# Optimization experiments

Hardware: AMD Instinct MI355X
Metric: run time of the kernel (lower is better)

## Reference

```python
import jax, jax.numpy as jnp
import numpy as np

B, S, D, H, F, E, K = 4, 2048, 1024, 16, 4096, 8, 2
HD = D // H
TEMP = 1.0
EPS = 1e-5


def _layernorm(x, g, b):
    mu = jnp.mean(x, axis=-1, keepdims=True)
    var = jnp.mean((x - mu) ** 2, axis=-1, keepdims=True)
    return (x - mu) * jax.lax.rsqrt(var + EPS) * g + b


def setup_inputs() -> dict:
    key = jax.random.key(0)
    ks = jax.random.split(key, 20)
    sd = 1.0 / np.sqrt(D)
    sf = 1.0 / np.sqrt(F)
    inp = {
        'x': jax.random.normal(ks[0], (B, S, D), jnp.float32),
        'Wq': jax.random.normal(ks[1], (D, D), jnp.float32) * sd,
        'bq': jnp.zeros((D,), jnp.float32),
        'Wk': jax.random.normal(ks[2], (D, D), jnp.float32) * sd,
        'bk': jnp.zeros((D,), jnp.float32),
        'Wv': jax.random.normal(ks[3], (D, D), jnp.float32) * sd,
        'bv': jnp.zeros((D,), jnp.float32),
        'Wo': jax.random.normal(ks[4], (D, D), jnp.float32) * sd,
        'bo': jnp.zeros((D,), jnp.float32),
        'g1': jnp.ones((D,), jnp.float32),
        'beta1': jnp.zeros((D,), jnp.float32),
        'gateW': jax.random.normal(ks[5], (D, E), jnp.float32) * sd,
        'gateb': jnp.zeros((E,), jnp.float32),
        'eW1': jax.random.normal(ks[6], (E, D, F), jnp.float32) * sd,
        'eb1': jnp.zeros((E, F), jnp.float32),
        'eW2': jax.random.normal(ks[7], (E, F, D), jnp.float32) * sf,
        'eb2': jnp.zeros((E, D), jnp.float32),
        'g2': jnp.ones((D,), jnp.float32),
        'beta2': jnp.zeros((D,), jnp.float32),
    }
    return inp


def _forward(x, Wq, bq, Wk, bk, Wv, bv, Wo, bo, g1, beta1, gateW, gateb, eW1, eb1, eW2, eb2, g2, beta2):
    # ---- multi-head self-attention ----
    q = (x @ Wq + bq).reshape(B, S, H, HD).transpose(0, 2, 1, 3)  # [B,H,S,HD]
    k = (x @ Wk + bk).reshape(B, S, H, HD).transpose(0, 2, 1, 3)
    v = (x @ Wv + bv).reshape(B, S, H, HD).transpose(0, 2, 1, 3)
    scores = jnp.einsum('bhqd,bhkd->bhqk', q, k) / np.sqrt(HD)
    attn = jax.nn.softmax(scores, axis=-1)
    out = jnp.einsum('bhqk,bhkd->bhqd', attn, v)
    out = out.transpose(0, 2, 1, 3).reshape(B, S, D) @ Wo + bo
    x = _layernorm(x + out, g1, beta1)

    # ---- MoE feed-forward with top-k routing ----
    T = B * S
    xf = x.reshape(T, D)
    gate_logits = (xf @ gateW + gateb) / TEMP
    gate_scores = jax.nn.softmax(gate_logits, axis=-1)            # [T,E]
    topk_scores, topk_idx = jax.lax.top_k(gate_scores, K)         # [T,K]
    topk_scores = topk_scores / jnp.sum(topk_scores, axis=-1, keepdims=True)
    # per-token combine weight for every expert: [T,E]
    w_full = jnp.zeros((T, E), xf.dtype).at[jnp.arange(T)[:, None], topk_idx].add(topk_scores)
    moe_out = jnp.zeros_like(xf)
    for e in range(E):  # small fixed expert count
        h = jax.nn.gelu(xf @ eW1[e] + eb1[e], approximate=False)
        y = h @ eW2[e] + eb2[e]
        moe_out = moe_out + w_full[:, e:e + 1] * y

    # ---- load-balancing auxiliary loss ----
    counts = jnp.sum(jax.nn.one_hot(topk_idx, E, dtype=xf.dtype), axis=(0, 1))  # [E]
    expert_fraction = counts / (T * K)
    routing_weights = jnp.mean(gate_scores, axis=0)
    aux_loss = E * jnp.sum(expert_fraction * routing_weights)

    x = _layernorm(x + moe_out.reshape(B, S, D), g2, beta2)
    return x, aux_loss


def reference(x, Wq, bq, Wk, bk, Wv, bv, Wo, bo, g1, beta1, gateW, gateb, eW1, eb1, eW2, eb2, g2, beta2):
    return _forward(x, Wq, bq, Wk, bk, Wv, bv, Wo, bo, g1, beta1, gateW, gateb, eW1, eb1, eW2, eb2, g2, beta2)
```

## Files before the change

### kernel.cpp

```cpp
#include <hip/hip_runtime.h>
#include <math.h>

typedef unsigned short u16;
typedef __attribute__((ext_vector_type(8))) u16 u16x8;
typedef __attribute__((ext_vector_type(8))) __bf16 b16x8;
typedef __attribute__((ext_vector_type(4))) float f32x4;

#define DEV __device__ __forceinline__

namespace {

constexpr int Tc = 8192, Dc = 1024, Fc = 4096, Ec = 8;

DEV u16 f2bf(float f){ union{float f; unsigned u;} v; v.f=f; unsigned r = v.u + 0x7fffu + ((v.u>>16)&1u); return (u16)(r>>16); }
DEV float bf2f(u16 h){ union{unsigned u; float f;} v; v.u=((unsigned)h)<<16; return v.f; }
DEV f32x4 zero4(){ f32x4 z = {0.f,0.f,0.f,0.f}; return z; }
DEV f32x4 mfma16(u16x8 a, u16x8 b, f32x4 c){
  union { u16x8 u; b16x8 b; } ua, ub; ua.u = a; ub.u = b;
  return __builtin_amdgcn_mfma_f32_16x16x32_bf16(ua.b, ub.b, c, 0, 0, 0);
}
DEV float gelu_exact(float v){ return 0.5f*v*(1.0f + erff(v*0.70710678118654752f)); }

__global__ __launch_bounds__(256) void split_x_k(const float* __restrict__ x, u16* __restrict__ hi, u16* __restrict__ lo){
  size_t i = (size_t)blockIdx.x*256 + threadIdx.x;
  #pragma unroll
  for (int r=0;r<8;r++){
    size_t idx = i + (size_t)r*1048576;
    float v = x[idx];
    u16 h = f2bf(v);
    hi[idx] = h;
    lo[idx] = f2bf(v - bf2f(h));
  }
}

__global__ __launch_bounds__(256) void concat_bias_k(const float* __restrict__ bq, const float* __restrict__ bk,
                                                     const float* __restrict__ bv, float* __restrict__ dst){
  int n = blockIdx.x*256 + threadIdx.x;
  if (n < 3072) dst[n] = (n<1024) ? bq[n] : ((n<2048) ? bk[n-1024] : bv[n-2048]);
}

__global__ __launch_bounds__(256) void transpose_split_k(const float* __restrict__ W, u16* __restrict__ oHi, u16* __restrict__ oLo,
                                                         int Kd, int Nd, size_t inStride, size_t outStride){
  __shared__ float t[32][33];
  int e = blockIdx.z;
  W += (size_t)e*inStride; oHi += (size_t)e*outStride; if (oLo) oLo += (size_t)e*outStride;
  int k0 = blockIdx.x*32, n0 = blockIdx.y*32;
  int c = threadIdx.x & 31, r0 = threadIdx.x >> 5;
  #pragma unroll
  for (int i=0;i<4;i++){ int r = r0 + i*8; t[r][c] = W[(size_t)(k0+r)*Nd + n0 + c]; }
  __syncthreads();
  #pragma unroll
  for (int i=0;i<4;i++){
    int r = r0 + i*8;
    float v = t[c][r];
    size_t oidx = (size_t)(n0+r)*Kd + k0 + c;
    u16 h = f2bf(v);
    oHi[oidx] = h;
    if (oLo) oLo[oidx] = f2bf(v - bf2f(h));
  }
}

template<int MODE>
__global__ __launch_bounds__(256,2) void gemm_k(
    const u16* __restrict__ Ahi, const u16* __restrict__ Alo,
    const u16* __restrict__ Bhi, const u16* __restrict__ Blo,
    const float* __restrict__ bias,
    float* __restrict__ outF, u16* __restrict__ outHi, u16* __restrict__ outLo,
    const int* __restrict__ offsets,
    int N, int K, int lda, int ldb)
{
  constexpr bool X3 = (MODE <= 1);
  constexpr int PL = X3 ? 2 : 1;
  int Me = 0, rowbase = 0;
  if constexpr (MODE >= 2){
    int e = blockIdx.z;
    rowbase = offsets[e];
    Me = offsets[e+1] - rowbase;
    if ((int)blockIdx.x*128 >= Me) return;
    Ahi += (size_t)rowbase * lda;
    Bhi += (size_t)e * N * K;
    bias += (size_t)e * N;
  }
  __shared__ u16 sA[PL][128*40];
  __shared__ u16 sB[PL][128*40];
  const int tid = threadIdx.x;
  const int lane = tid & 63, wid = tid >> 6;
  const int l15 = lane & 15, l4 = lane >> 4;
  const int mh = (wid >> 1) * 64, nh = (wid & 1) * 64;
  const int bm = blockIdx.x, bn = blockIdx.y;

  f32x4 acc[4][4];
  #pragma unroll
  for (int i=0;i<4;i++)
    #pragma unroll
    for (int j=0;j<4;j++) acc[i][j] = zero4();

  const int nK = K >> 5;
  for (int kb=0; kb<nK; ++kb){
    const int k0 = kb << 5;
    __syncthreads();
    #pragma unroll
    for (int r2=0;r2<2;r2++){
      int c = tid + r2*256;
      int row = c >> 2, k8 = (c & 3) * 8;
      size_t ga = (size_t)(bm*128 + row)*lda + k0 + k8;
      size_t gb = (size_t)(bn*128 + row)*ldb + k0 + k8;
      *(u16x8*)&sA[0][row*40 + k8] = *(const u16x8*)(Ahi + ga);
      *(u16x8*)&sB[0][row*40 + k8] = *(const u16x8*)(Bhi + gb);
      if constexpr (X3){
        *(u16x8*)&sA[1][row*40 + k8] = *(const u16x8*)(Alo + ga);
        *(u16x8*)&sB[1][row*40 + k8] = *(const u16x8*)(Blo + gb);
      }
    }
    __syncthreads();
    u16x8 af[PL][4], bfr[PL][4];
    #pragma unroll
    for (int mt=0;mt<4;mt++){
      int ra = (mh + mt*16 + l15)*40 + l4*8;
      int rb = (nh + mt*16 + l15)*40 + l4*8;
      af[0][mt]  = *(const u16x8*)&sA[0][ra];
      bfr[0][mt] = *(const u16x8*)&sB[0][rb];
      if constexpr (X3){ af[1][mt] = *(const u16x8*)&sA[1][ra]; bfr[1][mt] = *(const u16x8*)&sB[1][rb]; }
    }
    #pragma unroll
    for (int mt=0;mt<4;mt++)
      #pragma unroll
      for (int nt=0;nt<4;nt++){
        acc[mt][nt] = mfma16(af[0][mt], bfr[0][nt], acc[mt][nt]);
        if constexpr (X3){
          acc[mt][nt] = mfma16(af[0][mt], bfr[1][nt], acc[mt][nt]);
          acc[mt][nt] = mfma16(af[1][mt], bfr[0][nt], acc[mt][nt]);
        }
      }
  }
  #pragma unroll
  for (int mt=0;mt<4;mt++)
    #pragma unroll
    for (int nt=0;nt<4;nt++)
      #pragma unroll
      for (int r=0;r<4;r++){
        int m = bm*128 + mh + mt*16 + l4*4 + r;
        int n = bn*128 + nh + nt*16 + l15;
        float v = acc[mt][nt][r];
        if constexpr (MODE == 0){
          v += bias[n];
          int which = n >> 10, h = (n >> 6) & 15, d = n & 63;
          int b = m >> 11, s = m & 2047;
          size_t idx = ((((size_t)which*4 + b)*16 + h)*2048 + s)*64 + d;
          u16 hi = f2bf(v);
          outHi[idx] = hi; outLo[idx] = f2bf(v - bf2f(hi));
        } else if constexpr (MODE == 1){
          outF[(size_t)m*1024 + n] = v + bias[n];
        } else if constexpr (MODE == 2){
          if (m < Me){
            float g = gelu_exact(v + bias[n]);
            outHi[(size_t)(rowbase + m)*N + n] = f2bf(g);
          }
        } else {
          if (m < Me){
            outHi[(size_t)(rowbase + m)*N + n] = f2bf(v + bias[n]);
          }
        }
      }
}

__global__ __launch_bounds__(256,2) void flash_k(
    const u16* __restrict__ qhi, const u16* __restrict__ qlo,
    const u16* __restrict__ khi, const u16* __restrict__ klo,
    const u16* __restrict__ vhi, const u16* __restrict__ vlo,
    u16* __restrict__ ohi, u16* __restrict__ olo)
{
  __shared__ u16 Kl[2][64*72];
  __shared__ u16 Vt[2][64*72];
  __shared__ u16 Pl[2][64*72];
  const int qt = blockIdx.x, bh = blockIdx.y;
  const int b = bh >> 4, h = bh & 15;
  const int tid = threadIdx.x, wid = tid >> 6, lane = tid & 63;
  const int l15 = lane & 15, l4 = lane >> 4;
  const size_t bhBase = (size_t)bh * (2048*64);

  u16x8 qf[2][2];
  #pragma unroll
  for (int ks=0;ks<2;ks++){
    size_t po = bhBase + (size_t)(qt*64 + wid*16 + l15)*64 + ks*32 + l4*8;
    qf[0][ks] = *(const u16x8*)(qhi + po);
    qf[1][ks] = *(const u16x8*)(qlo + po);
  }
  f32x4 O[4];
  #pragma unroll
  for (int nd=0;nd<4;nd++) O[nd] = zero4();
  float mrow[4], lrow[4];
  #pragma unroll
  for (int r=0;r<4;r++){ mrow[r] = -1e30f; lrow[r] = 0.f; }

  for (int t=0;t<32;++t){
    __syncthreads();
    const size_t kvBase = bhBase + (size_t)t*(64*64);
    #pragma unroll
    for (int pl=0; pl<2; ++pl){
      const u16* ks_ = pl ? klo : khi;
      const u16* vs_ = pl ? vlo : vhi;
      #pragma unroll
      for (int r2=0;r2<2;r2++){
        int c = tid + r2*256;
        int kk = c >> 3, c8 = (c & 7) * 8;
        *(u16x8*)&Kl[pl][kk*72 + c8] = *(const u16x8*)(ks_ + kvBase + (size_t)kk*64 + c8);
      }
      #pragma unroll
      for (int r2=0;r2<2;r2++){
        int c = tid + r2*256;
        int kk = c >> 3, d0 = (c & 7) * 8;
        u16x8 vv = *(const u16x8*)(vs_ + kvBase + (size_t)kk*64 + d0);
        #pragma unroll
        for (int j=0;j<8;j++) Vt[pl][(d0+j)*72 + kk] = vv[j];
      }
    }
    __syncthreads();

    f32x4 sc[4];
    #pragma unroll
    for (int nt=0;nt<4;nt++){
      u16x8 kf[2][2];
      #pragma unroll
      for (int pl=0;pl<2;pl++)
        #pragma unroll
        for (int ks=0;ks<2;ks++)
          kf[pl][ks] = *(const u16x8*)&Kl[pl][(nt*16 + l15)*72 + ks*32 + l4*8];
      f32x4 a = zero4();
      a = mfma16(qf[0][0], kf[0][0], a);
      a = mfma16(qf[0][1], kf[0][1], a);
      a = mfma16(qf[0][0], kf[1][0], a);
      a = mfma16(qf[0][1], kf[1][1], a);
      a = mfma16(qf[1][0], kf[0][0], a);
      a = mfma16(qf[1][1], kf[0][1], a);
      sc[nt] = a;
    }
    float alpha[4];
    #pragma unroll
    for (int r=0;r<4;r++){
      float mx = -1e30f;
      #pragma unroll
      for (int nt=0;nt<4;nt++){ sc[nt][r] *= 0.125f; mx = fmaxf(mx, sc[nt][r]); }
      #pragma unroll
      for (int sh=1; sh<16; sh<<=1) mx = fmaxf(mx, __shfl_xor(mx, sh, 64));
      float mn = fmaxf(mrow[r], mx);
      alpha[r] = __expf(mrow[r] - mn);
      mrow[r] = mn;
      float ls = 0.f;
      #pragma unroll
      for (int nt=0;nt<4;nt++){
        float p = __expf(sc[nt][r] - mn);
        sc[nt][r] = p;
        ls += p;
      }
      #pragma unroll
      for (int sh=1; sh<16; sh<<=1) ls += __shfl_xor(ls, sh, 64);
      lrow[r] = lrow[r]*alpha[r] + ls;
    }
    #pragma unroll
    for (int nt=0;nt<4;nt++)
      #pragma unroll
      for (int r=0;r<4;r++){
        int row = wid*16 + l4*4 + r;
        int col = nt*16 + l15;
        float p = sc[nt][r];
        u16 hi = f2bf(p);
        Pl[0][row*72 + col] = hi;
        Pl[1][row*72 + col] = f2bf(p - bf2f(hi));
      }
    #pragma unroll
    for (int nd=0;nd<4;nd++)
      #pragma unroll
      for (int r=0;r<4;r++) O[nd][r] *= alpha[r];
    u16x8 pf[2][2];
    #pragma unroll
    for (int pl=0;pl<2;pl++)
      #pragma unroll
      for (int ks=0;ks<2;ks++)
        pf[pl][ks] = *(const u16x8*)&Pl[pl][(wid*16 + l15)*72 + ks*32 + l4*8];
    #pragma unroll
    for (int nd=0;nd<4;nd++){
      u16x8 vf[2][2];
      #pragma unroll
      for (int pl=0;pl<2;pl++)
        #pragma unroll
        for (int ks=0;ks<2;ks++)
          vf[pl][ks] = *(const u16x8*)&Vt[pl][(nd*16 + l15)*72 + ks*32 + l4*8];
      f32x4 a = O[nd];
      a = mfma16(pf[0][0], vf[0][0], a);
      a = mfma16(pf[0][1], vf[0][1], a);
      a = mfma16(pf[0][0], vf[1][0], a);
      a = mfma16(pf[0][1], vf[1][1], a);
      a = mfma16(pf[1][0], vf[0][0], a);
      a = mfma16(pf[1][1], vf[0][1], a);
      O[nd] = a;
    }
  }
  #pragma unroll
  for (int nd=0;nd<4;nd++)
    #pragma unroll
    for (int r=0;r<4;r++){
      int srow = qt*64 + wid*16 + l4*4 + r;
      int d = nd*16 + l15;
      float v = O[nd][r] / lrow[r];
      size_t idx = ((size_t)b*2048 + srow)*1024 + h*64 + d;
      u16 hi = f2bf(v);
      ohi[idx] = hi; olo[idx] = f2bf(v - bf2f(hi));
    }
}

__global__ __launch_bounds__(256) void ln1_k(const float* __restrict__ y1, const float* __restrict__ x,
                                             const float* __restrict__ g, const float* __restrict__ be,
                                             float* __restrict__ x1, u16* __restrict__ x1b){
  __shared__ float red[2][4];
  int t = blockIdx.x, tid = threadIdx.x;
  const float* yr = y1 + (size_t)t*1024;
  const float* xr = x + (size_t)t*1024;
  float v[4], s = 0.f, s2 = 0.f;
  #pragma unroll
  for (int i=0;i<4;i++){ int d = tid + i*256; v[i] = yr[d] + xr[d]; s += v[i]; s2 += v[i]*v[i]; }
  #pragma unroll
  for (int sh=1; sh<64; sh<<=1){ s += __shfl_xor(s, sh, 64); s2 += __shfl_xor(s2, sh, 64); }
  int wid = tid >> 6, lane = tid & 63;
  if (lane == 0){ red[0][wid] = s; red[1][wid] = s2; }
  __syncthreads();
  s  = red[0][0]+red[0][1]+red[0][2]+red[0][3];
  s2 = red[1][0]+red[1][1]+red[1][2]+red[1][3];
  float mu = s * (1.f/1024.f);
  float var = s2 * (1.f/1024.f) - mu*mu;
  float inv = 1.0f / sqrtf(var + 1e-5f);
  #pragma unroll
  for (int i=0;i<4;i++){
    int d = tid + i*256;
    float o2 = (v[i]-mu)*inv*g[d] + be[d];
    x1[(size_t)t*1024 + d] = o2;
    x1b[(size_t)t*1024 + d] = f2bf(o2);
  }
}

__global__ __launch_bounds__(256) void ln2_k(const float* __restrict__ x1, const u16* __restrict__ ybuf,
                                             const int* __restrict__ tok_slot, const float* __restrict__ tok_wt,
                                             const float* __restrict__ g, const float* __restrict__ be,
                                             float* __restrict__ out){
  __shared__ float red[2][4];
  int t = blockIdx.x, tid = threadIdx.x;
  int s0 = tok_slot[t*2], s1 = tok_slot[t*2+1];
  float w0 = tok_wt[t*2], w1 = tok_wt[t*2+1];
  const float* xr = x1 + (size_t)t*1024;
  const u16* y0 = ybuf + (size_t)s0*1024;
  const u16* y1p = ybuf + (size_t)s1*1024;
  float v[4], s = 0.f, s2 = 0.f;
  #pragma unroll
  for (int i=0;i<4;i++){
    int d = tid + i*256;
    v[i] = xr[d] + w0*bf2f(y0[d]) + w1*bf2f(y1p[d]);
    s += v[i]; s2 += v[i]*v[i];
  }
  #pragma unroll
  for (int sh=1; sh<64; sh<<=1){ s += __shfl_xor(s, sh, 64); s2 += __shfl_xor(s2, sh, 64); }
  int wid = tid >> 6, lane = tid & 63;
  if (lane == 0){ red[0][wid] = s; red[1][wid] = s2; }
  __syncthreads();
  s  = red[0][0]+red[0][1]+red[0][2]+red[0][3];
  s2 = red[1][0]+red[1][1]+red[1][2]+red[1][3];
  float mu = s * (1.f/1024.f);
  float var = s2 * (1.f/1024.f) - mu*mu;
  float inv = 1.0f / sqrtf(var + 1e-5f);
  #pragma unroll
  for (int i=0;i<4;i++){
    int d = tid + i*256;
    out[(size_t)t*1024 + d] = (v[i]-mu)*inv*g[d] + be[d];
  }
}

__global__ __launch_bounds__(256) void gate_k(const float* __restrict__ x1, const float* __restrict__ gW, const float* __restrict__ gb,
                                              int* __restrict__ tok_e, float* __restrict__ tok_wt,
                                              int* __restrict__ counts, float* __restrict__ probsum){
  __shared__ float psum[8];
  __shared__ int pcnt[8];
  int tid = threadIdx.x, wid = tid>>6, lane = tid&63;
  if (tid < 8){ psum[tid] = 0.f; pcnt[tid] = 0; }
  __syncthreads();
  for (int it=0; it<8; ++it){
    int t = blockIdx.x*32 + wid*8 + it;
    const float* xr = x1 + (size_t)t*1024;
    float a0=0,a1=0,a2=0,a3=0,a4=0,a5=0,a6=0,a7=0;
    #pragma unroll
    for (int j=0;j<16;j++){
      int i = lane + j*64;
      float xv = xr[i];
      const float4* w4 = (const float4*)(gW + (size_t)i*8);
      float4 wa = w4[0], wb = w4[1];
      a0 += xv*wa.x; a1 += xv*wa.y; a2 += xv*wa.z; a3 += xv*wa.w;
      a4 += xv*wb.x; a5 += xv*wb.y; a6 += xv*wb.z; a7 += xv*wb.w;
    }
    #pragma unroll
    for (int sh=1; sh<64; sh<<=1){
      a0 += __shfl_xor(a0,sh,64); a1 += __shfl_xor(a1,sh,64); a2 += __shfl_xor(a2,sh,64); a3 += __shfl_xor(a3,sh,64);
      a4 += __shfl_xor(a4,sh,64); a5 += __shfl_xor(a5,sh,64); a6 += __shfl_xor(a6,sh,64); a7 += __shfl_xor(a7,sh,64);
    }
    if (lane == 0){
      float lg[8] = {a0+gb[0],a1+gb[1],a2+gb[2],a3+gb[3],a4+gb[4],a5+gb[5],a6+gb[6],a7+gb[7]};
      float mx = lg[0];
      #pragma unroll
      for (int e=1;e<8;e++) mx = fmaxf(mx, lg[e]);
      float pex[8], sum = 0.f;
      #pragma unroll
      for (int e=0;e<8;e++){ pex[e] = __expf(lg[e]-mx); sum += pex[e]; }
      int e0 = 0; float b0v = lg[0];
      #pragma unroll
      for (int e=1;e<8;e++) if (lg[e] > b0v){ b0v = lg[e]; e0 = e; }
      int e1 = -1; float b1v = -1e30f;
      #pragma unroll
      for (int e=0;e<8;e++) if (e != e0 && lg[e] > b1v){ b1v = lg[e]; e1 = e; }
      float rr = __expf(b1v - b0v);
      float w0 = 1.f/(1.f+rr), w1 = rr/(1.f+rr);
      tok_e[t*2] = e0; tok_e[t*2+1] = e1;
      tok_wt[t*2] = w0; tok_wt[t*2+1] = w1;
      atomicAdd(&pcnt[e0], 1); atomicAdd(&pcnt[e1], 1);
      float isum = 1.f/sum;
      #pragma unroll
      for (int e=0;e<8;e++) atomicAdd(&psum[e], pex[e]*isum);
    }
  }
  __syncthreads();
  if (tid < 8){ atomicAdd(&counts[tid], pcnt[tid]); atomicAdd(&probsum[tid], psum[tid]); }
}

__global__ void offsets_k(const int* __restrict__ counts, int* __restrict__ offsets){
  if (threadIdx.x == 0 && blockIdx.x == 0){
    int o = 0;
    for (int e=0;e<8;e++){ offsets[e] = o; o += counts[e]; }
    offsets[8] = o;
  }
}

__global__ __launch_bounds__(256) void assign_k(const int* __restrict__ tok_e, const int* __restrict__ offsets,
                                                int* __restrict__ cursor, int* __restrict__ slot_tok,
                                                int* __restrict__ tok_slot){
  int t = blockIdx.x*256 + threadIdx.x;
  #pragma unroll
  for (int k2=0;k2<2;k2++){
    int e = tok_e[t*2+k2];
    int pos = atomicAdd(&cursor[e], 1);
    int slot = offsets[e] + pos;
    slot_tok[slot] = t;
    tok_slot[t*2+k2] = slot;
  }
}

__global__ __launch_bounds__(256) void gather_k(const u16* __restrict__ x1b, const int* __restrict__ slot_tok, u16* __restrict__ xg){
  int slot = blockIdx.x*4 + (threadIdx.x >> 6);
  int lane = threadIdx.x & 63;
  int t = slot_tok[slot];
  const u16x8* src = (const u16x8*)(x1b + (size_t)t*1024);
  u16x8* dst = (u16x8*)(xg + (size_t)slot*1024);
  dst[lane] = src[lane];
  dst[lane + 64] = src[lane + 64];
}

__global__ void aux_k(const int* __restrict__ counts, const float* __restrict__ probsum, float* __restrict__ outAux){
  if (threadIdx.x == 0 && blockIdx.x == 0){
    float s = 0.f;
    for (int e=0;e<8;e++){
      float frac = (float)counts[e] * (1.f/16384.f);
      float rw = probsum[e] * (1.f/8192.f);
      s += frac * rw;
    }
    outAux[0] = 8.f * s;
  }
}

}

extern "C" void kernel_launch(void* const* d_in, const int* in_sizes, int n_in,
                              void* d_out, int out_size, void* d_ws, size_t ws_size,
                              hipStream_t stream)
{
  (void)in_sizes; (void)n_in; (void)out_size;
  const float* x   = (const float*)d_in[0];
  const float* Wq  = (const float*)d_in[1];
  const float* bq  = (const float*)d_in[2];
  const float* Wk  = (const float*)d_in[3];
  const float* bk  = (const float*)d_in[4];
  const float* Wv  = (const float*)d_in[5];
  const float* bv  = (const float*)d_in[6];
  const float* Wo  = (const float*)d_in[7];
  const float* bo  = (const float*)d_in[8];
  const float* g1  = (const float*)d_in[9];
  const float* be1 = (const float*)d_in[10];
  const float* gW  = (const float*)d_in[11];
  const float* gb  = (const float*)d_in[12];
  const float* eW1 = (const float*)d_in[13];
  const float* eb1 = (const float*)d_in[14];
  const float* eW2 = (const float*)d_in[15];
  const float* eb2 = (const float*)d_in[16];
  const float* g2  = (const float*)d_in[17];
  const float* be2 = (const float*)d_in[18];
  float* out = (float*)d_out;

  char* base = (char*)d_ws;
  size_t o = 0;
  auto take = [&](size_t bytes){ size_t r = o; o = (o + bytes + 255) & ~(size_t)255; return r; };
  const size_t SZbf = (size_t)Tc*Dc*2;
  size_t o_xhi  = take(SZbf);
  size_t o_xlo  = take(SZbf);
  size_t o_wqh  = take((size_t)3072*1024*2);
  size_t o_wql  = take((size_t)3072*1024*2);
  size_t o_qkvh = take(3*SZbf);
  size_t o_qkvl = take(3*SZbf);
  size_t o_e1t = 0;
  size_t o_e2t = (size_t)Ec*Dc*Fc*2;
  size_t o_woh = take((size_t)1024*1024*2);
  size_t o_wol = take((size_t)1024*1024*2);
  size_t o_att = take((size_t)16512*1024*2);
  size_t o_y1  = take((size_t)Tc*Dc*4);
  size_t o_x1  = take((size_t)Tc*Dc*4);
  size_t o_x1b = take(SZbf);
  size_t o_h   = take((size_t)16512*Fc*2);
  size_t o_yb  = take((size_t)16512*Dc*2);
  size_t o_ctl = take(1<<20);
  if (ws_size < o) return;

  int*   counts   = (int*)(base + o_ctl + 0);
  int*   cursor   = (int*)(base + o_ctl + 64);
  int*   offs     = (int*)(base + o_ctl + 128);
  float* probsum  = (float*)(base + o_ctl + 192);
  float* bqkv     = (float*)(base + o_ctl + 1024);
  int*   tok_e    = (int*)(base + o_ctl + 16384);
  float* tok_wt   = (float*)(base + o_ctl + 16384 + 65536);
  int*   tok_slot = (int*)(base + o_ctl + 16384 + 131072);
  int*   slot_tok = (int*)(base + o_ctl + 16384 + 196608);

  hipMemsetAsync(base + o_ctl, 0, 256, stream);
  concat_bias_k<<<dim3(12),dim3(256),0,stream>>>(bq, bk, bv, bqkv);
  split_x_k<<<dim3(4096),dim3(256),0,stream>>>(x, (u16*)(base+o_xhi), (u16*)(base+o_xlo));
  transpose_split_k<<<dim3(32,32,1),dim3(256),0,stream>>>(Wq, (u16*)(base+o_wqh),              (u16*)(base+o_wql),              1024,1024, 0,0);
  transpose_split_k<<<dim3(32,32,1),dim3(256),0,stream>>>(Wk, (u16*)(base+o_wqh)+1024*1024,    (u16*)(base+o_wql)+1024*1024,    1024,1024, 0,0);
  transpose_split_k<<<dim3(32,32,1),dim3(256),0,stream>>>(Wv, (u16*)(base+o_wqh)+2*1024*1024,  (u16*)(base+o_wql)+2*1024*1024,  1024,1024, 0,0);
  transpose_split_k<<<dim3(32,32,1),dim3(256),0,stream>>>(Wo, (u16*)(base+o_woh), (u16*)(base+o_wol), 1024,1024, 0,0);

  gemm_k<0><<<dim3(64,24),dim3(256),0,stream>>>((u16*)(base+o_xhi),(u16*)(base+o_xlo),(u16*)(base+o_wqh),(u16*)(base+o_wql),
      bqkv, nullptr, (u16*)(base+o_qkvh), (u16*)(base+o_qkvl), nullptr, 3072, 1024, 1024, 1024);

  {
    u16* qh = (u16*)(base+o_qkvh); u16* ql = (u16*)(base+o_qkvl);
    flash_k<<<dim3(32,64),dim3(256),0,stream>>>(qh, ql, qh+8388608, ql+8388608, qh+16777216, ql+16777216,
        (u16*)(base+o_att), (u16*)(base+o_att)+8388608);
  }

  transpose_split_k<<<dim3(32,128,8),dim3(256),0,stream>>>(eW1, (u16*)(base+o_e1t), nullptr, 1024, 4096, (size_t)1024*4096, (size_t)4096*1024);
  transpose_split_k<<<dim3(128,32,8),dim3(256),0,stream>>>(eW2, (u16*)(base+o_e2t), nullptr, 4096, 1024, (size_t)4096*1024, (size_t)1024*4096);

  gemm_k<1><<<dim3(64,8),dim3(256),0,stream>>>((u16*)(base+o_att),(u16*)(base+o_att)+8388608,(u16*)(base+o_woh),(u16*)(base+o_wol),
      bo, (float*)(base+o_y1), nullptr, nullptr, nullptr, 1024, 1024, 1024, 1024);

  ln1_k<<<dim3(8192),dim3(256),0,stream>>>((float*)(base+o_y1), x, g1, be1, (float*)(base+o_x1), (u16*)(base+o_x1b));
  gate_k<<<dim3(256),dim3(256),0,stream>>>((float*)(base+o_x1), gW, gb, tok_e, tok_wt, counts, probsum);
  offsets_k<<<dim3(1),dim3(64),0,stream>>>(counts, offs);
  assign_k<<<dim3(32),dim3(256),0,stream>>>(tok_e, offs, cursor, slot_tok, tok_slot);
  gather_k<<<dim3(4096),dim3(256),0,stream>>>((u16*)(base+o_x1b), slot_tok, (u16*)(base+o_att));

  gemm_k<2><<<dim3(64,32,8),dim3(256),0,stream>>>((u16*)(base+o_att), nullptr, (u16*)(base+o_e1t), nullptr,
      eb1, nullptr, (u16*)(base+o_h), nullptr, offs, 4096, 1024, 1024, 1024);
  gemm_k<3><<<dim3(64,8,8),dim3(256),0,stream>>>((u16*)(base+o_h), nullptr, (u16*)(base+o_e2t), nullptr,
      eb2, nullptr, (u16*)(base+o_yb), nullptr, offs, 1024, 4096, 4096, 4096);

  ln2_k<<<dim3(8192),dim3(256),0,stream>>>((float*)(base+o_x1), (u16*)(base+o_yb), tok_slot, tok_wt, g2, be2, out);
  aux_k<<<dim3(1),dim3(64),0,stream>>>(counts, probsum, out + (size_t)Tc*Dc);
}
```

Baseline: 2.130 ms.

## Use direct global-to-LDS loads in GEMM, pre-transpose V, and double flash query tile

The GEMM now fills shared memory with global_load_lds 16-byte copies into an unpadded 32-wide tile, in place of register-staged stores into a padded layout. The QKV projection writes V already transposed, so the flash kernel loads V rows straight into LDS instead of scattering them element by element. Each flash block now handles 128 queries instead of 64, reusing every K/V tile load across twice as many rows. The P hi/lo planes are packed into one 32-bit word and split back with perm instructions. The unpadded GEMM tile may cause LDS bank conflicts, and the larger flash tile raises register pressure under the (256,2) launch bounds.

Result: faster. 1.977 ms (-7.2%).

```diff
diff --git a/kernel.cpp b/kernel.cpp
--- a/kernel.cpp
+++ b/kernel.cpp
@@ -2,6 +2,7 @@
 #include <math.h>
 
 typedef unsigned short u16;
+typedef unsigned int u32;
 typedef __attribute__((ext_vector_type(8))) u16 u16x8;
 typedef __attribute__((ext_vector_type(8))) __bf16 b16x8;
 typedef __attribute__((ext_vector_type(4))) float f32x4;
@@ -20,6 +21,12 @@
   return __builtin_amdgcn_mfma_f32_16x16x32_bf16(ua.b, ub.b, c, 0, 0, 0);
 }
 DEV float gelu_exact(float v){ return 0.5f*v*(1.0f + erff(v*0.70710678118654752f)); }
+
+typedef __attribute__((address_space(1))) const unsigned GU;
+typedef __attribute__((address_space(3))) unsigned LU;
+DEV void cp16(const u16* g, u16* l){
+  __builtin_amdgcn_global_load_lds((GU*)g, (LU*)l, 16, 0, 0);
+}
 
 __global__ __launch_bounds__(256) void split_x_k(const float* __restrict__ x, u16* __restrict__ hi, u16* __restrict__ lo){
   size_t i = (size_t)blockIdx.x*256 + threadIdx.x;
@@ -81,13 +88,15 @@
     Bhi += (size_t)e * N * K;
     bias += (size_t)e * N;
   }
-  __shared__ u16 sA[PL][128*40];
-  __shared__ u16 sB[PL][128*40];
+  __shared__ u16 sA[PL][128*32];
+  __shared__ u16 sB[PL][128*32];
   const int tid = threadIdx.x;
   const int lane = tid & 63, wid = tid >> 6;
   const int l15 = lane & 15, l4 = lane >> 4;
   const int mh = (wid >> 1) * 64, nh = (wid & 1) * 64;
   const int bm = blockIdx.x, bn = blockIdx.y;
+  const int srow = lane >> 2;
+  const int sk8  = (lane & 3) * 8;
 
   f32x4 acc[4][4];
   #pragma unroll
@@ -100,24 +109,24 @@
     const int k0 = kb << 5;
     __syncthreads();
     #pragma unroll
-    for (int r2=0;r2<2;r2++){
-      int c = tid + r2*256;
-      int row = c >> 2, k8 = (c & 3) * 8;
-      size_t ga = (size_t)(bm*128 + row)*lda + k0 + k8;
-      size_t gb = (size_t)(bn*128 + row)*ldb + k0 + k8;
-      *(u16x8*)&sA[0][row*40 + k8] = *(const u16x8*)(Ahi + ga);
-      *(u16x8*)&sB[0][row*40 + k8] = *(const u16x8*)(Bhi + gb);
+    for (int c=0;c<2;c++){
+      int chunk = wid*2 + c;
+      int row = chunk*16 + srow;
+      size_t ga = (size_t)(bm*128 + row)*lda + k0 + sk8;
+      size_t gb = (size_t)(bn*128 + row)*ldb + k0 + sk8;
+      cp16(Ahi + ga, &sA[0][chunk*512]);
+      cp16(Bhi + gb, &sB[0][chunk*512]);
       if constexpr (X3){
-        *(u16x8*)&sA[1][row*40 + k8] = *(const u16x8*)(Alo + ga);
-        *(u16x8*)&sB[1][row*40 + k8] = *(const u16x8*)(Blo + gb);
+        cp16(Alo + ga, &sA[1][chunk*512]);
+        cp16(Blo + gb, &sB[1][chunk*512]);
       }
     }
     __syncthreads();
     u16x8 af[PL][4], bfr[PL][4];
     #pragma unroll
     for (int mt=0;mt<4;mt++){
-      int ra = (mh + mt*16 + l15)*40 + l4*8;
-      int rb = (nh + mt*16 + l15)*40 + l4*8;
+      int ra = (mh + mt*16 + l15)*32 + l4*8;
+      int rb = (nh + mt*16 + l15)*32 + l4*8;
       af[0][mt]  = *(const u16x8*)&sA[0][ra];
       bfr[0][mt] = *(const u16x8*)&sB[0][rb];
       if constexpr (X3){ af[1][mt] = *(const u16x8*)&sA[1][ra]; bfr[1][mt] = *(const u16x8*)&sB[1][rb]; }
@@ -146,7 +155,11 @@
           v += bias[n];
           int which = n >> 10, h = (n >> 6) & 15, d = n & 63;
           int b = m >> 11, s = m & 2047;
-          size_t idx = ((((size_t)which*4 + b)*16 + h)*2048 + s)*64 + d;
+          size_t idx;
+          if (which == 2)
+            idx = ((((size_t)2*4 + b)*16 + h)*64 + d)*2048 + s;
+          else
+            idx = ((((size_t)which*4 + b)*16 + h)*2048 + s)*64 + d;
           u16 hi = f2bf(v);
           outHi[idx] = hi; outLo[idx] = f2bf(v - bf2f(hi));
         } else if constexpr (MODE == 1){
@@ -167,117 +180,137 @@
 __global__ __launch_bounds__(256,2) void flash_k(
     const u16* __restrict__ qhi, const u16* __restrict__ qlo,
     const u16* __restrict__ khi, const u16* __restrict__ klo,
-    const u16* __restrict__ vhi, const u16* __restrict__ vlo,
+    const u16* __restrict__ vthi, const u16* __restrict__ vtlo,
     u16* __restrict__ ohi, u16* __restrict__ olo)
 {
   __shared__ u16 Kl[2][64*72];
   __shared__ u16 Vt[2][64*72];
-  __shared__ u16 Pl[2][64*72];
+  __shared__ u32 Pint[128*68];
   const int qt = blockIdx.x, bh = blockIdx.y;
   const int b = bh >> 4, h = bh & 15;
   const int tid = threadIdx.x, wid = tid >> 6, lane = tid & 63;
   const int l15 = lane & 15, l4 = lane >> 4;
   const size_t bhBase = (size_t)bh * (2048*64);
 
-  u16x8 qf[2][2];
-  #pragma unroll
-  for (int ks=0;ks<2;ks++){
-    size_t po = bhBase + (size_t)(qt*64 + wid*16 + l15)*64 + ks*32 + l4*8;
-    qf[0][ks] = *(const u16x8*)(qhi + po);
-    qf[1][ks] = *(const u16x8*)(qlo + po);
-  }
-  f32x4 O[4];
-  #pragma unroll
-  for (int nd=0;nd<4;nd++) O[nd] = zero4();
-  float mrow[4], lrow[4];
-  #pragma unroll
-  for (int r=0;r<4;r++){ mrow[r] = -1e30f; lrow[r] = 0.f; }
+  u16x8 qf[2][2][2];
+  #pragma unroll
+  for (int mi=0;mi<2;mi++)
+    #pragma unroll
+    for (int ks=0;ks<2;ks++){
+      size_t po = bhBase + (size_t)(qt*128 + wid*32 + mi*16 + l15)*64 + ks*32 + l4*8;
+      qf[mi][0][ks] = *(const u16x8*)(qhi + po);
+      qf[mi][1][ks] = *(const u16x8*)(qlo + po);
+    }
+  f32x4 O[2][4];
+  #pragma unroll
+  for (int mi=0;mi<2;mi++)
+    #pragma unroll
+    for (int nd=0;nd<4;nd++) O[mi][nd] = zero4();
+  float mrow[2][4], lrow[2][4];
+  #pragma unroll
+  for (int mi=0;mi<2;mi++)
+    #pragma unroll
+    for (int r=0;r<4;r++){ mrow[mi][r] = -1e30f; lrow[mi][r] = 0.f; }
 
   for (int t=0;t<32;++t){
     __syncthreads();
-    const size_t kvBase = bhBase + (size_t)t*(64*64);
+    const size_t kBase = bhBase + (size_t)t*(64*64);
     #pragma unroll
     for (int pl=0; pl<2; ++pl){
-      const u16* ks_ = pl ? klo : khi;
-      const u16* vs_ = pl ? vlo : vhi;
+      const u16* kp = pl ? klo : khi;
+      const u16* vp = pl ? vtlo : vthi;
       #pragma unroll
       for (int r2=0;r2<2;r2++){
         int c = tid + r2*256;
-        int kk = c >> 3, c8 = (c & 7) * 8;
-        *(u16x8*)&Kl[pl][kk*72 + c8] = *(const u16x8*)(ks_ + kvBase + (size_t)kk*64 + c8);
-      }
-      #pragma unroll
-      for (int r2=0;r2<2;r2++){
-        int c = tid + r2*256;
-        int kk = c >> 3, d0 = (c & 7) * 8;
-        u16x8 vv = *(const u16x8*)(vs_ + kvBase + (size_t)kk*64 + d0);
-        #pragma unroll
-        for (int j=0;j<8;j++) Vt[pl][(d0+j)*72 + kk] = vv[j];
+        int rr = c >> 3, c8 = (c & 7) * 8;
+        *(u16x8*)&Kl[pl][rr*72 + c8] = *(const u16x8*)(kp + kBase + (size_t)rr*64 + c8);
+        *(u16x8*)&Vt[pl][rr*72 + c8] = *(const u16x8*)(vp + bhBase + (size_t)rr*2048 + t*64 + c8);
       }
     }
     __syncthreads();
 
-    f32x4 sc[4];
-    #pragma unroll
-    for (int nt=0;nt<4;nt++){
-      u16x8 kf[2][2];
+    u16x8 kf[4][2][2];
+    #pragma unroll
+    for (int nt=0;nt<4;nt++)
       #pragma unroll
       for (int pl=0;pl<2;pl++)
         #pragma unroll
         for (int ks=0;ks<2;ks++)
-          kf[pl][ks] = *(const u16x8*)&Kl[pl][(nt*16 + l15)*72 + ks*32 + l4*8];
-      f32x4 a = zero4();
-      a = mfma16(qf[0][0], kf[0][0], a);
-      a = mfma16(qf[0][1], kf[0][1], a);
-      a = mfma16(qf[0][0], kf[1][0], a);
-      a = mfma16(qf[0][1], kf[1][1], a);
-      a = mfma16(qf[1][0], kf[0][0], a);
-      a = mfma16(qf[1][1], kf[0][1], a);
-      sc[nt] = a;
-    }
-    float alpha[4];
-    #pragma unroll
-    for (int r=0;r<4;r++){
-      float mx = -1e30f;
-      #pragma unroll
-      for (int nt=0;nt<4;nt++){ sc[nt][r] *= 0.125f; mx = fmaxf(mx, sc[nt][r]); }
-      #pragma unroll
-      for (int sh=1; sh<16; sh<<=1) mx = fmaxf(mx, __shfl_xor(mx, sh, 64));
-      float mn = fmaxf(mrow[r], mx);
-      alpha[r] = __expf(mrow[r] - mn);
-      mrow[r] = mn;
-      float ls = 0.f;
+          kf[nt][pl][ks] = *(const u16x8*)&Kl[pl][(nt*16 + l15)*72 + ks*32 + l4*8];
+
+    #pragma unroll
+    for (int mi=0;mi<2;mi++){
+      f32x4 sc[4];
       #pragma unroll
       for (int nt=0;nt<4;nt++){
-        float p = __expf(sc[nt][r] - mn);
-        sc[nt][r] = p;
-        ls += p;
-      }
-      #pragma unroll
-      for (int sh=1; sh<16; sh<<=1) ls += __shfl_xor(ls, sh, 64);
-      lrow[r] = lrow[r]*alpha[r] + ls;
-    }
-    #pragma unroll
-    for (int nt=0;nt<4;nt++)
+        f32x4 a = zero4();
+        a = mfma16(qf[mi][0][0], kf[nt][0][0], a);
+        a = mfma16(qf[mi][0][1], kf[nt][0][1], a);
+        a = mfma16(qf[mi][0][0], kf[nt][1][0], a);
+        a = mfma16(qf[mi][0][1], kf[nt][1][1], a);
+        a = mfma16(qf[mi][1][0], kf[nt][0][0], a);
+        a = mfma16(qf[mi][1][1], kf[nt][0][1], a);
+        sc[nt] = a;
+      }
+      float alpha[4];
       #pragma unroll
       for (int r=0;r<4;r++){
-        int row = wid*16 + l4*4 + r;
-        int col = nt*16 + l15;
-        float p = sc[nt][r];
-        u16 hi = f2bf(p);
-        Pl[0][row*72 + col] = hi;
-        Pl[1][row*72 + col] = f2bf(p - bf2f(hi));
-      }
-    #pragma unroll
-    for (int nd=0;nd<4;nd++)
-      #pragma unroll
-      for (int r=0;r<4;r++) O[nd][r] *= alpha[r];
-    u16x8 pf[2][2];
-    #pragma unroll
-    for (int pl=0;pl<2;pl++)
-      #pragma unroll
-      for (int ks=0;ks<2;ks++)
-        pf[pl][ks] = *(const u16x8*)&Pl[pl][(wid*16 + l15)*72 + ks*32 + l4*8];
+        float mx = -1e30f;
+        #pragma unroll
+        for (int nt=0;nt<4;nt++){ sc[nt][r] *= 0.125f; mx = fmaxf(mx, sc[nt][r]); }
+        #pragma unroll
+        for (int sh=1; sh<16; sh<<=1) mx = fmaxf(mx, __shfl_xor(mx, sh, 64));
+        float mn = fmaxf(mrow[mi][r], mx);
+        alpha[r] = __expf(mrow[mi][r] - mn);
+        mrow[mi][r] = mn;
+        float ls = 0.f;
+        #pragma unroll
+        for (int nt=0;nt<4;nt++){
+          float p = __expf(sc[nt][r] - mn);
+          sc[nt][r] = p;
+          ls += p;
+        }
+        #pragma unroll
+        for (int sh=1; sh<16; sh<<=1) ls += __shfl_xor(ls, sh, 64);
+        lrow[mi][r] = lrow[mi][r]*alpha[r] + ls;
+      }
+      #pragma unroll
+      for (int nt=0;nt<4;nt++)
+        #pragma unroll
+        for (int r=0;r<4;r++){
+          int row = wid*32 + mi*16 + l4*4 + r;
+          int col = nt*16 + l15;
+          float p = sc[nt][r];
+          u16 hi = f2bf(p);
+          u16 lo = f2bf(p - bf2f(hi));
+          Pint[row*68 + col] = (u32)hi | ((u32)lo << 16);
+        }
+      #pragma unroll
+      for (int nd=0;nd<4;nd++)
+        #pragma unroll
+        for (int r=0;r<4;r++) O[mi][nd][r] *= alpha[r];
+    }
+
+    u16x8 pf[2][2][2];
+    #pragma unroll
+    for (int mi=0;mi<2;mi++)
+      #pragma unroll
+      for (int ks=0;ks<2;ks++){
+        const u32* pr = &Pint[(wid*32 + mi*16 + l15)*68 + ks*32 + l4*8];
+        uint4 c0 = *(const uint4*)pr;
+        uint4 c1 = *(const uint4*)(pr + 4);
+        union { u16x8 v; u32 u[4]; } ph, pl2;
+        ph.u[0]  = __builtin_amdgcn_perm(c0.y, c0.x, 0x05040100u);
+        ph.u[1]  = __builtin_amdgcn_perm(c0.w, c0.z, 0x05040100u);
+        ph.u[2]  = __builtin_amdgcn_perm(c1.y, c1.x, 0x05040100u);
+        ph.u[3]  = __builtin_amdgcn_perm(c1.w, c1.z, 0x05040100u);
+        pl2.u[0] = __builtin_amdgcn_perm(c0.y, c0.x, 0x07060302u);
+        pl2.u[1] = __builtin_amdgcn_perm(c0.w, c0.z, 0x07060302u);
+        pl2.u[2] = __builtin_amdgcn_perm(c1.y, c1.x, 0x07060302u);
+        pl2.u[3] = __builtin_amdgcn_perm(c1.w, c1.z, 0x07060302u);
+        pf[mi][0][ks] = ph.v;
+        pf[mi][1][ks] = pl2.v;
+      }
     #pragma unroll
     for (int nd=0;nd<4;nd++){
       u16x8 vf[2][2];
@@ -286,27 +319,32 @@
         #pragma unroll
         for (int ks=0;ks<2;ks++)
           vf[pl][ks] = *(const u16x8*)&Vt[pl][(nd*16 + l15)*72 + ks*32 + l4*8];
-      f32x4 a = O[nd];
-      a = mfma16(pf[0][0], vf[0][0], a);
-      a = mfma16(pf[0][1], vf[0][1], a);
-      a = mfma16(pf[0][0], vf[1][0], a);
-      a = mfma16(pf[0][1], vf[1][1], a);
-      a = mfma16(pf[1][0], vf[0][0], a);
-      a = mfma16(pf[1][1], vf[0][1], a);
-      O[nd] = a;
-    }
-  }
-  #pragma unroll
-  for (int nd=0;nd<4;nd++)
-    #pragma unroll
-    for (int r=0;r<4;r++){
-      int srow = qt*64 + wid*16 + l4*4 + r;
-      int d = nd*16 + l15;
-      float v = O[nd][r] / lrow[r];
-      size_t idx = ((size_t)b*2048 + srow)*1024 + h*64 + d;
-      u16 hi = f2bf(v);
-      ohi[idx] = hi; olo[idx] = f2bf(v - bf2f(hi));
-    }
+      #pragma unroll
+      for (int mi=0;mi<2;mi++){
+        f32x4 a = O[mi][nd];
+        a = mfma16(pf[mi][0][0], vf[0][0], a);
+        a = mfma16(pf[mi][0][1], vf[0][1], a);
+        a = mfma16(pf[mi][0][0], vf[1][0], a);
+        a = mfma16(pf[mi][0][1], vf[1][1], a);
+        a = mfma16(pf[mi][1][0], vf[0][0], a);
+        a = mfma16(pf[mi][1][1], vf[0][1], a);
+        O[mi][nd] = a;
+      }
+    }
+  }
+  #pragma unroll
+  for (int mi=0;mi<2;mi++)
+    #pragma unroll
+    for (int nd=0;nd<4;nd++)
+      #pragma unroll
+      for (int r=0;r<4;r++){
+        int srow = qt*128 + wid*32 + mi*16 + l4*4 + r;
+        int d = nd*16 + l15;
+        float v = O[mi][nd][r] / lrow[mi][r];
+        size_t idx = ((size_t)b*2048 + srow)*1024 + h*64 + d;
+        u16 hi = f2bf(v);
+        ohi[idx] = hi; olo[idx] = f2bf(v - bf2f(hi));
+      }
 }
 
 __global__ __launch_bounds__(256) void ln1_k(const float* __restrict__ y1, const float* __restrict__ x,
@@ -545,7 +583,7 @@
 
   {
     u16* qh = (u16*)(base+o_qkvh); u16* ql = (u16*)(base+o_qkvl);
-    flash_k<<<dim3(32,64),dim3(256),0,stream>>>(qh, ql, qh+8388608, ql+8388608, qh+16777216, ql+16777216,
+    flash_k<<<dim3(16,64),dim3(256),0,stream>>>(qh, ql, qh+8388608, ql+8388608, qh+16777216, ql+16777216,
         (u16*)(base+o_att), (u16*)(base+o_att)+8388608);
   }
 
```
